# Kernel optimization log

Measured on AMD Instinct MI355X. Metric: run time of the kernel, lower is better.

## Reference

```python
import jax, jax.numpy as jnp
import numpy as np

N = 256
DOT = 512      # dot_num
HC = 16        # 128 // 8
WC = 128       # 1024 // 8
THRED = 1.0


def setup_inputs() -> dict:
    key = jax.random.key(0)
    k1, k2 = jax.random.split(key)
    x = jax.random.normal(k1, (N, 1, 1), dtype=jnp.float32)
    W = jax.random.normal(k2, (2 * DOT, 1), dtype=jnp.float32)  # Linear(1, 1024) weight [out,in]
    return {"x": x, "W": W}


def reference(x, W):
    # in_layer: Linear(1, 1024, bias=False) + Tanh
    fc_res = jnp.tanh(jnp.matmul(x, W.T))          # [N, 1, 1024]
    point_set = fc_res.reshape(N, DOT, 2) / 2 + 0.5  # [N, 512, 2], range [0,1]
    x_set = point_set[:, :, 0] * WC                # [N, 512]
    y_set = point_set[:, :, 1] * HC                # [N, 512]
    # coordinate grids, broadcast against [N, 512, 1, 1]
    h = jnp.arange(HC, dtype=jnp.float32)[None, None, :, None]   # [1,1,16,1]
    w = jnp.arange(WC, dtype=jnp.float32)[None, None, None, :]   # [1,1,1,128]
    dx = w - x_set[:, :, None, None]               # [N,512,16,128]
    dy = h - y_set[:, :, None, None]
    dis_mat = jnp.sqrt(dx * dx + dy * dy)
    weight_mat = jax.nn.relu((THRED - dis_mat) * 3)
    lumi_val = jnp.tanh(jnp.sum(weight_mat, axis=1, keepdims=True))  # [N,1,16,128]
    return lumi_val * 2 - 1
```

## Files before the change

### kernel.cpp

```cpp
#include <hip/hip_runtime.h>

#define NB   256
#define DOT  512
#define HC   16
#define WC   128

__global__ __launch_bounds__(256) void gen_kernel(const float* __restrict__ x,
                                                  const float* __restrict__ W,
                                                  float* __restrict__ out) {
    __shared__ float acc[HC * WC];
    const int n   = blockIdx.x;
    const int tid = threadIdx.x;
    const float xn = x[n];

    #pragma unroll
    for (int i = 0; i < 8; ++i) acc[tid + i * 256] = 0.0f;
    __syncthreads();

    #pragma unroll
    for (int pp = 0; pp < 2; ++pp) {
        const int d = tid + pp * 256;
        const float2 w2 = ((const float2*)W)[d];
        const float px = (tanhf(xn * w2.x) * 0.5f + 0.5f) * (float)WC;
        const float py = (tanhf(xn * w2.y) * 0.5f + 0.5f) * (float)HC;
        const int wc0 = (int)px;
        const int hc0 = (int)py;
        #pragma unroll
        for (int dh = -1; dh <= 1; ++dh) {
            const int h = hc0 + dh;
            if (h < 0 || h >= HC) continue;
            const float fy = (float)h - py;
            #pragma unroll
            for (int dw = -1; dw <= 1; ++dw) {
                const int w = wc0 + dw;
                if (w < 0 || w >= WC) continue;
                const float fx = (float)w - px;
                const float d2 = fx * fx + fy * fy;
                if (d2 < 1.0f) {
                    const float val = (1.0f - sqrtf(d2)) * 3.0f;
                    atomicAdd(&acc[h * WC + w], val);
                }
            }
        }
    }
    __syncthreads();

    float4* o4 = (float4*)(out + n * (HC * WC));
    const float4* a4 = (const float4*)acc;
    #pragma unroll
    for (int v = 0; v < 2; ++v) {
        const int idx = tid + v * 256;
        float4 a = a4[idx];
        float4 r;
        r.x = tanhf(a.x) * 2.0f - 1.0f;
        r.y = tanhf(a.y) * 2.0f - 1.0f;
        r.z = tanhf(a.z) * 2.0f - 1.0f;
        r.w = tanhf(a.w) * 2.0f - 1.0f;
        o4[idx] = r;
    }
}

extern "C" void kernel_launch(void* const* d_in, const int* in_sizes, int n_in,
                              void* d_out, int out_size, void* d_ws, size_t ws_size,
                              hipStream_t stream) {
    const float* x = (const float*)d_in[0];
    const float* W = (const float*)d_in[1];
    float* out = (float*)d_out;
    gen_kernel<<<NB, 256, 0, stream>>>(x, W, out);
}
```

Before: 58.77 us.

## Use 512 threads, replicated shared accumulators, and fast tanh

Launches 512 threads per block so each thread handles one point instead of two. Splits the shared accumulator into four replicas, chosen by thread id, to reduce atomic contention, and sums the replicas in the epilogue. Replaces tanhf with an exp plus reciprocal approximation. This costs more shared memory, adds a four-way reduction, and introduces small precision risk from the fast tanh.

```diff
diff --git a/kernel.cpp b/kernel.cpp
--- a/kernel.cpp
+++ b/kernel.cpp
@@ -1,63 +1,64 @@
 #include <hip/hip_runtime.h>
 
-#define NB   256
-#define DOT  512
-#define HC   16
-#define WC   128
+#define NB      256
+#define DOT     512
+#define HC      16
+#define WC      128
+#define CELLS   (HC * WC)
+#define NREP    4
+#define RSTRIDE (CELLS + 8)
 
-__global__ __launch_bounds__(256) void gen_kernel(const float* __restrict__ x,
+__device__ __forceinline__ float fast_tanh(float v) {
+    float e = __expf(2.0f * v);
+    return 1.0f - 2.0f * __builtin_amdgcn_rcpf(e + 1.0f);
+}
+
+__global__ __launch_bounds__(512) void gen_kernel(const float* __restrict__ x,
                                                   const float* __restrict__ W,
                                                   float* __restrict__ out) {
-    __shared__ float acc[HC * WC];
+    __shared__ float acc[NREP * RSTRIDE];
     const int n   = blockIdx.x;
     const int tid = threadIdx.x;
     const float xn = x[n];
 
-    #pragma unroll
-    for (int i = 0; i < 8; ++i) acc[tid + i * 256] = 0.0f;
+    for (int i = tid; i < NREP * RSTRIDE; i += 512) acc[i] = 0.0f;
     __syncthreads();
 
+    const float2 w2 = ((const float2*)W)[tid];
+    const float px = (fast_tanh(xn * w2.x) * 0.5f + 0.5f) * (float)WC;
+    const float py = (fast_tanh(xn * w2.y) * 0.5f + 0.5f) * (float)HC;
+    const int wc0 = (int)px;
+    const int hc0 = (int)py;
+    float* myacc = acc + (tid & (NREP - 1)) * RSTRIDE;
     #pragma unroll
-    for (int pp = 0; pp < 2; ++pp) {
-        const int d = tid + pp * 256;
-        const float2 w2 = ((const float2*)W)[d];
-        const float px = (tanhf(xn * w2.x) * 0.5f + 0.5f) * (float)WC;
-        const float py = (tanhf(xn * w2.y) * 0.5f + 0.5f) * (float)HC;
-        const int wc0 = (int)px;
-        const int hc0 = (int)py;
+    for (int dh = -1; dh <= 1; ++dh) {
+        const int h = hc0 + dh;
+        if (h < 0 || h >= HC) continue;
+        const float fy = (float)h - py;
         #pragma unroll
-        for (int dh = -1; dh <= 1; ++dh) {
-            const int h = hc0 + dh;
-            if (h < 0 || h >= HC) continue;
-            const float fy = (float)h - py;
-            #pragma unroll
-            for (int dw = -1; dw <= 1; ++dw) {
-                const int w = wc0 + dw;
-                if (w < 0 || w >= WC) continue;
-                const float fx = (float)w - px;
-                const float d2 = fx * fx + fy * fy;
-                if (d2 < 1.0f) {
-                    const float val = (1.0f - sqrtf(d2)) * 3.0f;
-                    atomicAdd(&acc[h * WC + w], val);
-                }
+        for (int dw = -1; dw <= 1; ++dw) {
+            const int w = wc0 + dw;
+            if (w < 0 || w >= WC) continue;
+            const float fx = (float)w - px;
+            const float d2 = fx * fx + fy * fy;
+            if (d2 < 1.0f) {
+                atomicAdd(&myacc[h * WC + w], (1.0f - sqrtf(d2)) * 3.0f);
             }
         }
     }
     __syncthreads();
 
-    float4* o4 = (float4*)(out + n * (HC * WC));
-    const float4* a4 = (const float4*)acc;
-    #pragma unroll
-    for (int v = 0; v < 2; ++v) {
-        const int idx = tid + v * 256;
-        float4 a = a4[idx];
-        float4 r;
-        r.x = tanhf(a.x) * 2.0f - 1.0f;
-        r.y = tanhf(a.y) * 2.0f - 1.0f;
-        r.z = tanhf(a.z) * 2.0f - 1.0f;
-        r.w = tanhf(a.w) * 2.0f - 1.0f;
-        o4[idx] = r;
-    }
+    const int c = tid * 4;
+    const float4 a0 = *(const float4*)&acc[0 * RSTRIDE + c];
+    const float4 a1 = *(const float4*)&acc[1 * RSTRIDE + c];
+    const float4 a2 = *(const float4*)&acc[2 * RSTRIDE + c];
+    const float4 a3 = *(const float4*)&acc[3 * RSTRIDE + c];
+    float4 r;
+    r.x = fast_tanh(a0.x + a1.x + a2.x + a3.x) * 2.0f - 1.0f;
+    r.y = fast_tanh(a0.y + a1.y + a2.y + a3.y) * 2.0f - 1.0f;
+    r.z = fast_tanh(a0.z + a1.z + a2.z + a3.z) * 2.0f - 1.0f;
+    r.w = fast_tanh(a0.w + a1.w + a2.w + a3.w) * 2.0f - 1.0f;
+    ((float4*)(out + n * CELLS))[tid] = r;
 }
 
 extern "C" void kernel_launch(void* const* d_in, const int* in_sizes, int n_in,
@@ -66,5 +67,5 @@
     const float* x = (const float*)d_in[0];
     const float* W = (const float*)d_in[1];
     float* out = (float*)d_out;
-    gen_kernel<<<NB, 256, 0, stream>>>(x, W, out);
+    gen_kernel<<<NB, 512, 0, stream>>>(x, W, out);
 }
```

Result: no change. 58.00 us (-1.3%).
